# Kernel optimization log

Hardware: AMD Instinct MI355X
Metric: run time of the kernel (lower is better)

## Reference

```python
import jax, jax.numpy as jnp
import numpy as np

TEMP = 0.1
EPS = 1e-08

def _l2norm(x):
    # F.normalize semantics: x / max(||x||, 1e-12)
    n = jnp.linalg.norm(x, axis=-1, keepdims=True)
    return x / jnp.maximum(n, 1e-12)

def setup_inputs() -> dict:
    key = jax.random.key(0)
    k0, k1, k2, k3, k4 = jax.random.split(key, 5)
    B, Ph, Pw, D, O = 32, 32, 32, 512, 128
    P = Ph * Pw
    patch_features = jax.random.normal(k0, (B, Ph, Pw, D), jnp.float32)
    obj_features = jax.random.normal(k1, (B, O, D), jnp.float32)
    # e1i: each patch positively matched to one object (one-hot rows)
    idx = jax.random.randint(k2, (B, P), 0, O)
    e1i = jax.nn.one_hot(idx, O, dtype=jnp.float32)
    # e1j / e2j: sparse binary negative masks
    e1j = (jax.random.uniform(k3, (B, P, P)) < 0.1).astype(jnp.float32)
    e2j = (jax.random.uniform(k4, (B, P, O)) < 0.1).astype(jnp.float32)
    return {"patch_features": patch_features, "obj_features": obj_features,
            "e1i": e1i, "e1j": e1j, "e2j": e2j}

def reference(patch_features, obj_features, e1i, e1j, e2j):
    B, D = patch_features.shape[0], patch_features.shape[-1]
    pf = patch_features.reshape(B, -1, D)          # [B, P, D]
    pn = _l2norm(pf)
    on = _l2norm(obj_features)                     # [B, O, D]
    po_sim = jnp.einsum('bpd,bod->bpo', pn, on)    # patch-object cosine sim
    po_exp = jnp.exp(po_sim / TEMP)
    pp_exp = jnp.exp(jnp.einsum('bpd,bqd->bpq', pn, pn) / TEMP)
    delta_E1i_E2i = jnp.sum(e1i * po_exp, axis=-1)     # [B, P]
    sum_E1i_E1j = jnp.sum(e1j * pp_exp, axis=-1)
    sum_E1i_E2j = jnp.sum(e2j * po_exp, axis=-1)
    ratio = delta_E1i_E2i / (delta_E1i_E2i + sum_E1i_E1j + sum_E1i_E2j + EPS)
    loss_all = -jnp.log(ratio + EPS)                   # [B, P]
    valid = (jnp.sum(e1i, axis=-1) > 0).astype(loss_all.dtype)  # [B, P]
    n_valid = jnp.sum(valid)
    loss = jnp.sum(loss_all * valid) / n_valid
    matched = jnp.argmax(po_sim, axis=-1)              # [B, P]
    labels = jnp.take_along_axis(e1i, matched[..., None], axis=-1)[..., 0]
    matched_success_ratio = jnp.sum(labels * valid) / n_valid
    return loss, matched_success_ratio
```

## Files before the change

### kernel.cpp

```cpp
#include <hip/hip_runtime.h>
#include <hip/hip_bf16.h>

constexpr int BB = 32;
constexpr int P  = 1024;
constexpr int O  = 128;
constexpr int D  = 512;
constexpr float EPS = 1e-8f;
constexpr float SCL = 14.426950408889634f;

typedef __attribute__((ext_vector_type(8))) short short8;
typedef __attribute__((ext_vector_type(16))) float f32x16;

__device__ __forceinline__ unsigned short f2bf(float f) {
  __hip_bfloat16 h = __float2bfloat16(f);
  unsigned short u;
  __builtin_memcpy(&u, &h, sizeof(u));
  return u;
}

__device__ __forceinline__ void gld_lds16(const void* g, void* l) {
  __builtin_amdgcn_global_load_lds(
      (const __attribute__((address_space(1))) void*)g,
      (__attribute__((address_space(3))) void*)l, 16, 0, 0);
}

__global__ __launch_bounds__(256) void prep_kernel(
    const float* __restrict__ pf, const float* __restrict__ of,
    __hip_bfloat16* __restrict__ pn, __hip_bfloat16* __restrict__ on) {
  int lane = threadIdx.x & 63;
  int row = blockIdx.x * 4 + (threadIdx.x >> 6);
  const float* src;
  __hip_bfloat16* dst;
  if (row < BB * P) {
    src = pf + (size_t)row * D;
    dst = pn + (size_t)row * D;
  } else {
    int r = row - BB * P;
    if (r >= BB * O) return;
    src = of + (size_t)r * D;
    dst = on + (size_t)r * D;
  }
  float4 v0 = *(const float4*)(src + lane * 8);
  float4 v1 = *(const float4*)(src + lane * 8 + 4);
  float ss = v0.x * v0.x + v0.y * v0.y + v0.z * v0.z + v0.w * v0.w +
             v1.x * v1.x + v1.y * v1.y + v1.z * v1.z + v1.w * v1.w;
  #pragma unroll
  for (int s = 1; s < 64; s <<= 1) ss += __shfl_xor(ss, s);
  float sc = 1.0f / fmaxf(sqrtf(ss), 1e-12f);
  short8 w;
  w[0] = (short)f2bf(v0.x * sc); w[1] = (short)f2bf(v0.y * sc);
  w[2] = (short)f2bf(v0.z * sc); w[3] = (short)f2bf(v0.w * sc);
  w[4] = (short)f2bf(v1.x * sc); w[5] = (short)f2bf(v1.y * sc);
  w[6] = (short)f2bf(v1.z * sc); w[7] = (short)f2bf(v1.w * sc);
  *reinterpret_cast<short8*>(dst + lane * 8) = w;
}

__global__ __launch_bounds__(512, 4) void icl_main5(
    const __hip_bfloat16* __restrict__ pn, const __hip_bfloat16* __restrict__ on,
    const float* __restrict__ e1i, const float* __restrict__ e1j,
    const float* __restrict__ e2j,
    float* __restrict__ d_row, float* __restrict__ s1_row,
    float* __restrict__ s2_row, unsigned long long* __restrict__ pk_row,
    int* __restrict__ ip_row) {

  __shared__ __hip_bfloat16 Bs[64 * 64 * 8];

  const int tid  = threadIdx.x;
  const int l    = tid & 63;
  const int wid  = tid >> 6;
  const int half = l >> 5;
  const int l31  = l & 31;

  const int bid    = blockIdx.x;
  const int batch  = bid & 31;
  const int unit   = bid >> 5;
  const int stripe = unit >> 1;
  const int rh     = unit & 1;
  const bool isobj = stripe < 2;

  const __hip_bfloat16* pnb = pn + (size_t)batch * P * D;
  const __hip_bfloat16* onb = on + (size_t)batch * O * D;
  const __hip_bfloat16* bsrc =
      isobj ? onb + (size_t)stripe * 64 * D
            : pnb + (size_t)(stripe - 2) * 64 * D;

  #pragma unroll
  for (int i = 0; i < 8; ++i) {
    const int idx = i * 512 + tid;
    gld_lds16(bsrc + (size_t)(idx & 63) * D + (idx >> 6) * 8,
              (char*)Bs + (size_t)idx * 16);
  }
  __syncthreads();

  const int cb = stripe * 64;
  const int pb = (stripe - 2) * 64;

  for (int p = 0; p < 2; ++p) {
    const int rowt = rh * 512 + p * 256 + wid * 32;
    const __hip_bfloat16* a0 = pnb + (size_t)(rowt + l31) * D + half * 8;

    f32x16 acc0, acc1;
    #pragma unroll
    for (int k = 0; k < 16; ++k) { acc0[k] = 0.f; acc1[k] = 0.f; }

    #pragma unroll
    for (int s = 0; s < 32; ++s) {
      const char* bb = (const char*)Bs + (((s << 1) | half) << 10);
      short8 b0 = *reinterpret_cast<const short8*>(bb + (l31 << 4));
      short8 b1 = *reinterpret_cast<const short8*>(bb + ((32 + l31) << 4));
      short8 A0 = *reinterpret_cast<const short8*>(a0 + s * 16);
      acc0 = __builtin_amdgcn_mfma_f32_32x32x16_bf16(A0, b0, acc0, 0, 0, 0);
      acc1 = __builtin_amdgcn_mfma_f32_32x32x16_bf16(A0, b1, acc1, 0, 0, 0);
    }

    if (isobj) {
      #pragma unroll
      for (int r = 0; r < 16; ++r) {
        const int lrow = (r & 3) + ((r >> 2) << 3) + (half << 2);
        const size_t grow = (size_t)batch * P + rowt + lrow;
        const size_t gb = grow * O + cb;
        const int c0 = cb + l31, c1 = cb + 32 + l31;
        float s0 = acc0[r], s1v = acc1[r];
        float e0 = exp2f(s0 * SCL), e1 = exp2f(s1v * SCL);
        float m10 = e1i[gb + l31], m11 = e1i[gb + 32 + l31];
        float m20 = e2j[gb + l31], m21 = e2j[gb + 32 + l31];
        float dv  = m10 * e0 + m11 * e1;
        float s2v = m20 * e0 + m21 * e1;
        int ipv = (m11 > 0.5f) ? c1 : ((m10 > 0.5f) ? c0 : -1);
        float mvv; int miv;
        if (s1v > s0) { mvv = s1v; miv = c1; } else { mvv = s0; miv = c0; }
        #pragma unroll
        for (int s = 1; s < 32; s <<= 1) {
          dv  += __shfl_xor(dv, s);
          s2v += __shfl_xor(s2v, s);
          ipv  = max(ipv, __shfl_xor(ipv, s));
          float ov = __shfl_xor(mvv, s);
          int   oi = __shfl_xor(miv, s);
          if (ov > mvv || (ov == mvv && oi < miv)) { mvv = ov; miv = oi; }
        }
        if (l31 == 0) {
          if (dv != 0.f) atomicAdd(&d_row[grow], dv);
          atomicAdd(&s2_row[grow], s2v);
          unsigned long long pkv =
              ((unsigned long long)__float_as_uint(mvv + 2.0f) << 32) |
              (unsigned)(0xFFFFFFFFu - (unsigned)miv);
          atomicMax(&pk_row[grow], pkv);
          if (ipv >= 0) atomicMax(&ip_row[grow], ipv);
        }
      }
    } else {
      #pragma unroll
      for (int r = 0; r < 16; ++r) {
        const int lrow = (r & 3) + ((r >> 2) << 3) + (half << 2);
        const size_t grow = (size_t)batch * P + rowt + lrow;
        const size_t gb = grow * P + pb;
        float v = e1j[gb + l31] * exp2f(acc0[r] * SCL) +
                  e1j[gb + 32 + l31] * exp2f(acc1[r] * SCL);
        #pragma unroll
        for (int s = 1; s < 32; s <<= 1) v += __shfl_xor(v, s);
        if (l31 == 0) atomicAdd(&s1_row[grow], v);
      }
    }
  }
}

__global__ __launch_bounds__(256) void icl_reduce(
    const float* __restrict__ d_row, const float* __restrict__ s1_row,
    const float* __restrict__ s2_row, const unsigned long long* __restrict__ pk_row,
    const int* __restrict__ ip_row, float* __restrict__ accum) {
  __shared__ float red[12];
  const int tid = threadIdx.x;
  const int row = blockIdx.x * 256 + tid;
  float d = d_row[row], a = s1_row[row], c = s2_row[row];
  int ipv = ip_row[row];
  int miv = (int)(0xFFFFFFFFu - (unsigned)(pk_row[row] & 0xFFFFFFFFull));
  float valid = (ipv >= 0) ? 1.f : 0.f;
  float ratio = d / (d + a + c + EPS);
  float lsum = -logf(ratio + EPS) * valid;
  float lbl  = (ipv >= 0 && miv == ipv) ? 1.f : 0.f;
  float vct  = valid;
  #pragma unroll
  for (int s = 1; s < 64; s <<= 1) {
    lsum += __shfl_xor(lsum, s);
    lbl  += __shfl_xor(lbl, s);
    vct  += __shfl_xor(vct, s);
  }
  const int wid = tid >> 6;
  if ((tid & 63) == 0) {
    red[wid * 3 + 0] = lsum;
    red[wid * 3 + 1] = lbl;
    red[wid * 3 + 2] = vct;
  }
  __syncthreads();
  if (tid == 0) {
    atomicAdd(&accum[0], red[0] + red[3] + red[6] + red[9]);
    atomicAdd(&accum[1], red[1] + red[4] + red[7] + red[10]);
    atomicAdd(&accum[2], red[2] + red[5] + red[8] + red[11]);
  }
}

__global__ void finalize_kernel(const float* __restrict__ accum,
                                float* __restrict__ out) {
  if (threadIdx.x == 0 && blockIdx.x == 0) {
    float nv = accum[2];
    out[0] = accum[0] / nv;
    out[1] = accum[1] / nv;
  }
}

__global__ __launch_bounds__(256) void norm_kernel(
    const float* __restrict__ pf, const float* __restrict__ of,
    float* __restrict__ invp, float* __restrict__ invo) {
  int lane = threadIdx.x & 63;
  int row = blockIdx.x * 4 + (threadIdx.x >> 6);
  const float* src;
  float* dst;
  if (row < BB * P) {
    src = pf + (size_t)row * D;
    dst = invp + row;
  } else {
    int r = row - BB * P;
    if (r >= BB * O) return;
    src = of + (size_t)r * D;
    dst = invo + r;
  }
  float ss = 0.f;
  #pragma unroll
  for (int i = 0; i < 2; ++i) {
    float4 v = *(const float4*)(src + (lane + 64 * i) * 4);
    ss += v.x * v.x + v.y * v.y + v.z * v.z + v.w * v.w;
  }
  #pragma unroll
  for (int s = 1; s < 64; s <<= 1) ss += __shfl_xor(ss, s);
  if (lane == 0) *dst = 1.0f / fmaxf(sqrtf(ss), 1e-12f);
}

__global__ __launch_bounds__(256) void icl_main_v1(
    const float* __restrict__ pf, const float* __restrict__ of,
    const float* __restrict__ e1i, const float* __restrict__ e1j,
    const float* __restrict__ e2j, const float* __restrict__ invp,
    const float* __restrict__ invo, float* __restrict__ accum) {
  constexpr int PT = 128, BK = 64;
  __shared__ __hip_bfloat16 As[PT * BK];
  __shared__ __hip_bfloat16 Bs[PT * BK];
  __shared__ float d_l[2][PT], s2_l[2][PT], ei_l[2][PT], s1_l[2][PT], mv_l[2][PT];
  __shared__ int   mi_l[2][PT];
  __shared__ float red[12];

  const int tid  = threadIdx.x;
  const int lane = tid & 63;
  const int wid  = tid >> 6;
  const int wr   = wid >> 1;
  const int wc   = wid & 1;
  const int half = lane >> 5;
  const int l31  = lane & 31;
  const int b    = blockIdx.x & 31;
  const int pt   = blockIdx.x >> 5;
  const int row0 = pt * PT;

  const float* pfb = pf + (size_t)b * P * D;
  const float* ofb = of + (size_t)b * O * D;
  const float* ivp = invp + b * P + row0;
  const float* ivq = invp + b * P;
  const float* ivo = invo + b * O;

  float s1p[2][16];
  #pragma unroll
  for (int m = 0; m < 2; ++m)
    #pragma unroll
    for (int r = 0; r < 16; ++r) s1p[m][r] = 0.f;

  auto stage = [&](const float* __restrict__ src, const float* __restrict__ inv,
                   __hip_bfloat16* __restrict__ lds, int k0) {
    #pragma unroll
    for (int i = 0; i < 8; ++i) {
      int c = i * 256 + tid;
      int rr = c >> 4, kc = c & 15;
      float4 v = *(const float4*)(src + (size_t)rr * D + k0 + (kc << 2));
      float s = inv[rr];
      int off = rr * BK + ((((kc >> 1) ^ (rr & 7)) << 3) | ((kc & 1) << 2));
      ushort4 w;
      w.x = f2bf(v.x * s);
      w.y = f2bf(v.y * s);
      w.z = f2bf(v.z * s);
      w.w = f2bf(v.w * s);
      *reinterpret_cast<ushort4*>(lds + off) = w;
    }
  };

  for (int ct = 0; ct < 9; ++ct) {
    const float* bsrc = (ct == 0) ? ofb : pfb + (size_t)(ct - 1) * 128 * D;
    const float* binv = (ct == 0) ? ivo : ivq + (ct - 1) * 128;

    f32x16 acc[2][2];
    #pragma unroll
    for (int m = 0; m < 2; ++m)
      #pragma unroll
      for (int n = 0; n < 2; ++n)
        #pragma unroll
        for (int k = 0; k < 16; ++k) acc[m][n][k] = 0.f;

    for (int ks = 0; ks < D / BK; ++ks) {
      __syncthreads();
      stage(pfb + (size_t)row0 * D, ivp, As, ks * BK);
      stage(bsrc, binv, Bs, ks * BK);
      __syncthreads();
      #pragma unroll
      for (int kc = 0; kc < 4; ++kc) {
        short8 af[2], bfr[2];
        #pragma unroll
        for (int m = 0; m < 2; ++m) {
          int row = wr * 64 + m * 32 + l31;
          af[m] = *reinterpret_cast<const short8*>(
              As + row * BK + ((((kc << 1) | half) ^ (row & 7)) << 3));
        }
        #pragma unroll
        for (int n = 0; n < 2; ++n) {
          int col = wc * 64 + n * 32 + l31;
          bfr[n] = *reinterpret_cast<const short8*>(
              Bs + col * BK + ((((kc << 1) | half) ^ (col & 7)) << 3));
        }
        #pragma unroll
        for (int m = 0; m < 2; ++m)
          #pragma unroll
          for (int n = 0; n < 2; ++n)
            acc[m][n] = __builtin_amdgcn_mfma_f32_32x32x16_bf16(
                af[m], bfr[n], acc[m][n], 0, 0, 0);
      }
    }

    if (ct == 0) {
      #pragma unroll
      for (int m = 0; m < 2; ++m) {
        #pragma unroll
        for (int r = 0; r < 16; ++r) {
          int lrow = wr * 64 + m * 32 + (r & 3) + ((r >> 2) << 3) + (half << 2);
          size_t base = ((size_t)b * P + row0 + lrow) * O;
          float dsum = 0.f, s2s = 0.f, eis = 0.f, mval = -1e30f;
          int midx = 0;
          #pragma unroll
          for (int n = 0; n < 2; ++n) {
            int col = wc * 64 + n * 32 + l31;
            float sim = acc[m][n][r];
            float e = exp2f(sim * SCL);
            float v1 = e1i[base + col];
            float v2 = e2j[base + col];
            dsum += v1 * e;
            s2s  += v2 * e;
            eis  += v1;
            if (sim > mval) { mval = sim; midx = col; }
          }
          #pragma unroll
          for (int s = 1; s < 32; s <<= 1) {
            dsum += __shfl_xor(dsum, s);
            s2s  += __shfl_xor(s2s, s);
            eis  += __shfl_xor(eis, s);
            float ov = __shfl_xor(mval, s);
            int   oi = __shfl_xor(midx, s);
            if (ov > mval || (ov == mval && oi < midx)) { mval = ov; midx = oi; }
          }
          if (l31 == 0) {
            d_l[wc][lrow] = dsum;
            s2_l[wc][lrow] = s2s;
            ei_l[wc][lrow] = eis;
            mv_l[wc][lrow] = mval;
            mi_l[wc][lrow] = midx;
          }
        }
      }
    } else {
      const int qbase = (ct - 1) * 128;
      #pragma unroll
      for (int m = 0; m < 2; ++m) {
        #pragma unroll
        for (int r = 0; r < 16; ++r) {
          int lrow = wr * 64 + m * 32 + (r & 3) + ((r >> 2) << 3) + (half << 2);
          size_t base = ((size_t)b * P + row0 + lrow) * P + qbase;
          float s = 0.f;
          #pragma unroll
          for (int n = 0; n < 2; ++n) {
            int col = wc * 64 + n * 32 + l31;
            s += e1j[base + col] * exp2f(acc[m][n][r] * SCL);
          }
          s1p[m][r] += s;
        }
      }
    }
  }

  #pragma unroll
  for (int m = 0; m < 2; ++m) {
    #pragma unroll
    for (int r = 0; r < 16; ++r) {
      float v = s1p[m][r];
      #pragma unroll
      for (int s = 1; s < 32; s <<= 1) v += __shfl_xor(v, s);
      if (l31 == 0) {
        int lrow = wr * 64 + m * 32 + (r & 3) + ((r >> 2) << 3) + (half << 2);
        s1_l[wc][lrow] = v;
      }
    }
  }
  __syncthreads();

  float lsum = 0.f, lbl = 0.f, vct = 0.f;
  if (tid < PT) {
    float delta = d_l[0][tid] + d_l[1][tid];
    float s2 = s2_l[0][tid] + s2_l[1][tid];
    float eis = ei_l[0][tid] + ei_l[1][tid];
    float s1 = s1_l[0][tid] + s1_l[1][tid];
    float m0 = mv_l[0][tid], m1 = mv_l[1][tid];
    int mi = (m1 > m0) ? mi_l[1][tid] : mi_l[0][tid];
    float valid = (eis > 0.f) ? 1.f : 0.f;
    float ratio = delta / (delta + s1 + s2 + EPS);
    float loss = -logf(ratio + EPS);
    float label = e1i[((size_t)b * P + row0 + tid) * O + mi];
    lsum = loss * valid;
    lbl  = label * valid;
    vct  = valid;
  }
  #pragma unroll
  for (int s = 1; s < 64; s <<= 1) {
    lsum += __shfl_xor(lsum, s);
    lbl  += __shfl_xor(lbl, s);
    vct  += __shfl_xor(vct, s);
  }
  if (lane == 0) {
    red[wid * 3 + 0] = lsum;
    red[wid * 3 + 1] = lbl;
    red[wid * 3 + 2] = vct;
  }
  __syncthreads();
  if (tid == 0) {
    float a = red[0] + red[3] + red[6] + red[9];
    float c = red[1] + red[4] + red[7] + red[10];
    float v = red[2] + red[5] + red[8] + red[11];
    atomicAdd(&accum[0], a);
    atomicAdd(&accum[1], c);
    atomicAdd(&accum[2], v);
  }
}

extern "C" void kernel_launch(void* const* d_in, const int* in_sizes, int n_in,
                              void* d_out, int out_size, void* d_ws, size_t ws_size,
                              hipStream_t stream) {
  const float* pf  = (const float*)d_in[0];
  const float* of  = (const float*)d_in[1];
  const float* e1i = (const float*)d_in[2];
  const float* e1j = (const float*)d_in[3];
  const float* e2j = (const float*)d_in[4];

  char* base = (char*)d_ws;
  constexpr size_t NR = (size_t)BB * P;
  float* accum                 = (float*)base;
  float* d_row                 = (float*)(base + 64);
  float* s1_row                = (float*)(base + 64 + 4 * NR);
  float* s2_row                = (float*)(base + 64 + 8 * NR);
  unsigned long long* pk_row   = (unsigned long long*)(base + 64 + 12 * NR);
  int* ip_row                  = (int*)(base + 64 + 20 * NR);
  __hip_bfloat16* pn           = (__hip_bfloat16*)(base + 64 + 24 * NR);
  const size_t pn_bytes = (size_t)BB * P * D * 2;
  const size_t on_bytes = (size_t)BB * O * D * 2;
  __hip_bfloat16* on           = (__hip_bfloat16*)(base + 64 + 24 * NR + pn_bytes);
  const size_t need = 64 + 24 * NR + pn_bytes + on_bytes;

  if (ws_size >= need) {
    hipMemsetAsync(base, 0, 64 + 20 * NR, stream);
    hipMemsetAsync(ip_row, 0xFF, 4 * NR, stream);
    prep_kernel<<<(BB * P + BB * O) / 4, 256, 0, stream>>>(pf, of, pn, on);
    icl_main5<<<BB * 36, 512, 0, stream>>>(pn, on, e1i, e1j, e2j,
                                           d_row, s1_row, s2_row, pk_row, ip_row);
    icl_reduce<<<NR / 256, 256, 0, stream>>>(d_row, s1_row, s2_row, pk_row,
                                             ip_row, accum);
  } else {
    float* ws   = (float*)d_ws;
    float* invp = ws + 16;
    float* invo = ws + 16 + BB * P;
    hipMemsetAsync(accum, 0, 16 * sizeof(float), stream);
    norm_kernel<<<(BB * P + BB * O) / 4, 256, 0, stream>>>(pf, of, invp, invo);
    icl_main_v1<<<BB * (P / 128), 256, 0, stream>>>(pf, of, e1i, e1j, e2j,
                                                    invp, invo, accum);
  }
  finalize_kernel<<<1, 64, 0, stream>>>(accum, (float*)d_out);
}
```

Before: 181.0 us.

## Replace stripe-per-block GEMM with 128x128 LDS-tiled K-loop using swizzled A and B

Restructures the main kernel from blocks that hold a 64-column B stripe in LDS and stream A directly from global memory into 128x128 output tiles. Each block stages both A and B through XOR-swizzled LDS in 64-wide K chunks, and each of four waves computes a 2x2 set of 32x32 MFMA tiles. The goal is to cut redundant global A reads and raise operand reuse per wave. In exchange, the K loop now needs two barriers per step, has no double buffering, and the grid and block shape change (256 threads, 72 tiles per batch).

```diff
diff --git a/kernel.cpp b/kernel.cpp
--- a/kernel.cpp
+++ b/kernel.cpp
@@ -55,7 +55,7 @@
   *reinterpret_cast<short8*>(dst + lane * 8) = w;
 }
 
-__global__ __launch_bounds__(512, 4) void icl_main5(
+__global__ __launch_bounds__(256, 3) void icl_main7(
     const __hip_bfloat16* __restrict__ pn, const __hip_bfloat16* __restrict__ on,
     const float* __restrict__ e1i, const float* __restrict__ e1j,
     const float* __restrict__ e2j,
@@ -63,67 +63,92 @@
     float* __restrict__ s2_row, unsigned long long* __restrict__ pk_row,
     int* __restrict__ ip_row) {
 
-  __shared__ __hip_bfloat16 Bs[64 * 64 * 8];
+  __shared__ __hip_bfloat16 As[128 * 64];
+  __shared__ __hip_bfloat16 Bs[128 * 64];
 
   const int tid  = threadIdx.x;
   const int l    = tid & 63;
   const int wid  = tid >> 6;
+  const int wr   = wid >> 1;
+  const int wc   = wid & 1;
   const int half = l >> 5;
   const int l31  = l & 31;
 
-  const int bid    = blockIdx.x;
-  const int batch  = bid & 31;
-  const int unit   = bid >> 5;
-  const int stripe = unit >> 1;
-  const int rh     = unit & 1;
-  const bool isobj = stripe < 2;
+  const int bid   = blockIdx.x;
+  const int batch = bid & 31;
+  const int unit  = bid >> 5;
+  const int rt    = unit & 7;
+  const int ct    = unit >> 3;
+  const int row0  = rt * 128;
 
   const __hip_bfloat16* pnb = pn + (size_t)batch * P * D;
   const __hip_bfloat16* onb = on + (size_t)batch * O * D;
-  const __hip_bfloat16* bsrc =
-      isobj ? onb + (size_t)stripe * 64 * D
-            : pnb + (size_t)(stripe - 2) * 64 * D;
-
-  #pragma unroll
-  for (int i = 0; i < 8; ++i) {
-    const int idx = i * 512 + tid;
-    gld_lds16(bsrc + (size_t)(idx & 63) * D + (idx >> 6) * 8,
-              (char*)Bs + (size_t)idx * 16);
-  }
-  __syncthreads();
-
-  const int cb = stripe * 64;
-  const int pb = (stripe - 2) * 64;
-
-  for (int p = 0; p < 2; ++p) {
-    const int rowt = rh * 512 + p * 256 + wid * 32;
-    const __hip_bfloat16* a0 = pnb + (size_t)(rowt + l31) * D + half * 8;
-
-    f32x16 acc0, acc1;
-    #pragma unroll
-    for (int k = 0; k < 16; ++k) { acc0[k] = 0.f; acc1[k] = 0.f; }
-
-    #pragma unroll
-    for (int s = 0; s < 32; ++s) {
-      const char* bb = (const char*)Bs + (((s << 1) | half) << 10);
-      short8 b0 = *reinterpret_cast<const short8*>(bb + (l31 << 4));
-      short8 b1 = *reinterpret_cast<const short8*>(bb + ((32 + l31) << 4));
-      short8 A0 = *reinterpret_cast<const short8*>(a0 + s * 16);
-      acc0 = __builtin_amdgcn_mfma_f32_32x32x16_bf16(A0, b0, acc0, 0, 0, 0);
-      acc1 = __builtin_amdgcn_mfma_f32_32x32x16_bf16(A0, b1, acc1, 0, 0, 0);
-    }
-
-    if (isobj) {
+  const __hip_bfloat16* asrc = pnb + (size_t)row0 * D;
+  const __hip_bfloat16* bsrc = (ct == 0) ? onb : pnb + (size_t)(ct - 1) * 128 * D;
+
+  auto stage = [&](const __hip_bfloat16* __restrict__ src,
+                   __hip_bfloat16* __restrict__ lds, int k0) {
+    #pragma unroll
+    for (int i = 0; i < 4; ++i) {
+      int q = i * 256 + tid;
+      int rr = q >> 3, c = q & 7;
+      int gc = c ^ (rr & 7);
+      gld_lds16(src + (size_t)rr * D + k0 + (gc << 3),
+                (char*)lds + (size_t)(i * 256 + wid * 64) * 16);
+    }
+  };
+
+  f32x16 acc[2][2];
+  #pragma unroll
+  for (int m = 0; m < 2; ++m)
+    #pragma unroll
+    for (int n = 0; n < 2; ++n)
+      #pragma unroll
+      for (int k = 0; k < 16; ++k) acc[m][n][k] = 0.f;
+
+  for (int ks = 0; ks < 8; ++ks) {
+    __syncthreads();
+    stage(asrc, As, ks * 64);
+    stage(bsrc, Bs, ks * 64);
+    __syncthreads();
+    #pragma unroll
+    for (int kc = 0; kc < 4; ++kc) {
+      const int ch = (kc << 1) | half;
+      short8 af[2], bfr[2];
+      #pragma unroll
+      for (int m = 0; m < 2; ++m) {
+        int row = wr * 64 + m * 32 + l31;
+        af[m] = *reinterpret_cast<const short8*>(
+            As + row * 64 + ((ch ^ (row & 7)) << 3));
+      }
+      #pragma unroll
+      for (int n = 0; n < 2; ++n) {
+        int col = wc * 64 + n * 32 + l31;
+        bfr[n] = *reinterpret_cast<const short8*>(
+            Bs + col * 64 + ((ch ^ (col & 7)) << 3));
+      }
+      #pragma unroll
+      for (int m = 0; m < 2; ++m)
+        #pragma unroll
+        for (int n = 0; n < 2; ++n)
+          acc[m][n] = __builtin_amdgcn_mfma_f32_32x32x16_bf16(
+              af[m], bfr[n], acc[m][n], 0, 0, 0);
+    }
+  }
+
+  if (ct == 0) {
+    #pragma unroll
+    for (int m = 0; m < 2; ++m) {
       #pragma unroll
       for (int r = 0; r < 16; ++r) {
-        const int lrow = (r & 3) + ((r >> 2) << 3) + (half << 2);
-        const size_t grow = (size_t)batch * P + rowt + lrow;
-        const size_t gb = grow * O + cb;
-        const int c0 = cb + l31, c1 = cb + 32 + l31;
-        float s0 = acc0[r], s1v = acc1[r];
+        const int lrow = wr * 64 + m * 32 + (r & 3) + ((r >> 2) << 3) + (half << 2);
+        const size_t grow = (size_t)batch * P + row0 + lrow;
+        const size_t gb = grow * O;
+        const int c0 = wc * 64 + l31, c1 = wc * 64 + 32 + l31;
+        float s0 = acc[m][0][r], s1v = acc[m][1][r];
         float e0 = exp2f(s0 * SCL), e1 = exp2f(s1v * SCL);
-        float m10 = e1i[gb + l31], m11 = e1i[gb + 32 + l31];
-        float m20 = e2j[gb + l31], m21 = e2j[gb + 32 + l31];
+        float m10 = e1i[gb + c0], m11 = e1i[gb + c1];
+        float m20 = e2j[gb + c0], m21 = e2j[gb + c1];
         float dv  = m10 * e0 + m11 * e1;
         float s2v = m20 * e0 + m21 * e1;
         int ipv = (m11 > 0.5f) ? c1 : ((m10 > 0.5f) ? c0 : -1);
@@ -148,14 +173,19 @@
           if (ipv >= 0) atomicMax(&ip_row[grow], ipv);
         }
       }
-    } else {
+    }
+  } else {
+    const int pb = (ct - 1) * 128;
+    #pragma unroll
+    for (int m = 0; m < 2; ++m) {
       #pragma unroll
       for (int r = 0; r < 16; ++r) {
-        const int lrow = (r & 3) + ((r >> 2) << 3) + (half << 2);
-        const size_t grow = (size_t)batch * P + rowt + lrow;
+        const int lrow = wr * 64 + m * 32 + (r & 3) + ((r >> 2) << 3) + (half << 2);
+        const size_t grow = (size_t)batch * P + row0 + lrow;
         const size_t gb = grow * P + pb;
-        float v = e1j[gb + l31] * exp2f(acc0[r] * SCL) +
-                  e1j[gb + 32 + l31] * exp2f(acc1[r] * SCL);
+        const int c0 = wc * 64 + l31, c1 = wc * 64 + 32 + l31;
+        float v = e1j[gb + c0] * exp2f(acc[m][0][r] * SCL) +
+                  e1j[gb + c1] * exp2f(acc[m][1][r] * SCL);
         #pragma unroll
         for (int s = 1; s < 32; s <<= 1) v += __shfl_xor(v, s);
         if (l31 == 0) atomicAdd(&s1_row[grow], v);
@@ -468,7 +498,7 @@
     hipMemsetAsync(base, 0, 64 + 20 * NR, stream);
     hipMemsetAsync(ip_row, 0xFF, 4 * NR, stream);
     prep_kernel<<<(BB * P + BB * O) / 4, 256, 0, stream>>>(pf, of, pn, on);
-    icl_main5<<<BB * 36, 512, 0, stream>>>(pn, on, e1i, e1j, e2j,
+    icl_main7<<<BB * 72, 256, 0, stream>>>(pn, on, e1i, e1j, e2j,
                                            d_row, s1_row, s2_row, pk_row, ip_row);
     icl_reduce<<<NR / 256, 256, 0, stream>>>(d_row, s1_row, s2_row, pk_row,
                                              ip_row, accum);
```

After: 151.0 us. -16.5%, faster.
